# Kernel optimization log

Measured on AMD Instinct MI355X. Metric: run time of the kernel, lower is better.

The kernel has to match this reference:

```python
import jax, jax.numpy as jnp
import numpy as np

ROPE_BASE = 10000.0


def _rope_tables(T, d, dtype):
    # inv_freq over even indices, emb = concat(freqs, freqs) -> [T, d]
    inv_freq = 1.0 / (ROPE_BASE ** (jnp.arange(0, d, 2, dtype=jnp.float32) / d))
    t = jnp.arange(T, dtype=jnp.float32)
    freqs = jnp.einsum('i,j->ij', t, inv_freq)          # [T, d/2]
    emb = jnp.concatenate([freqs, freqs], axis=-1)      # [T, d]
    return jnp.cos(emb).astype(dtype), jnp.sin(emb).astype(dtype)


def _rotate_half(x):
    d = x.shape[-1] // 2
    return jnp.concatenate([-x[..., d:], x[..., :d]], axis=-1)


def _apply_rope(x, cos, sin):
    # x: [B, T, H, Dh]; cos/sin: [T, Dh] broadcast over batch and heads
    c = cos[None, :, None, :]
    s = sin[None, :, None, :]
    return x * c + _rotate_half(x) * s


def setup_inputs() -> dict:
    key = jax.random.key(0)
    k1, k2, k3 = jax.random.split(key, 3)
    B, T, C = 2, 2048, 1024
    x = jax.random.normal(k1, (B, T, C), dtype=jnp.float32)
    # weights stored as [in, out] (transposed nn.Linear), scaled like torch init
    W_qkv = jax.random.normal(k2, (C, 3 * C), dtype=jnp.float32) * (C ** -0.5)
    W_proj = jax.random.normal(k3, (C, C), dtype=jnp.float32) * (C ** -0.5)
    return {'x': x, 'W_qkv': W_qkv, 'W_proj': W_proj}


def reference(x, W_qkv, W_proj):
    B, T, C = x.shape
    H = 16
    Dh = C // H
    qkv = x @ W_qkv                                   # [B, T, 3C]
    q, k, v = jnp.split(qkv, 3, axis=-1)
    q = q.reshape(B, T, H, Dh)
    k = k.reshape(B, T, H, Dh)
    v = v.reshape(B, T, H, Dh)
    cos, sin = _rope_tables(T, Dh, x.dtype)
    q = _apply_rope(q, cos, sin)
    k = _apply_rope(k, cos, sin)
    scale = 1.0 / jnp.sqrt(jnp.asarray(Dh, dtype=x.dtype))
    # causal SDPA: scores [B, H, T, T]
    scores = jnp.einsum('bqhd,bkhd->bhqk', q, k) * scale
    causal = jnp.tril(jnp.ones((T, T), dtype=bool))
    scores = jnp.where(causal[None, None], scores, jnp.asarray(-jnp.inf, dtype=scores.dtype))
    attn = jax.nn.softmax(scores, axis=-1)
    y = jnp.einsum('bhqk,bkhd->bqhd', attn, v).reshape(B, T, C)
    return y @ W_proj
```

## Files before the change

### kernel.cpp

```cpp
#include <hip/hip_runtime.h>
#include <cstdint>
#include <cstddef>

typedef __bf16 bf16;
typedef __bf16 bf16x2 __attribute__((ext_vector_type(2)));
typedef __bf16 bf16x8 __attribute__((ext_vector_type(8)));
typedef float  f32x4  __attribute__((ext_vector_type(4)));

#define G2L(src, dst)                                                          \
  __builtin_amdgcn_global_load_lds(                                            \
      (const __attribute__((address_space(1))) unsigned int*)(src),            \
      (__attribute__((address_space(3))) unsigned int*)(dst), 16, 0, 0)

__global__ void k_f32_to_bf16(const float* __restrict__ in, bf16* __restrict__ out, int n) {
  int i = (blockIdx.x * blockDim.x + threadIdx.x) * 8;
  if (i >= n) return;
  float4 a = *(const float4*)(in + i);
  float4 b = *(const float4*)(in + i + 4);
  bf16x8 o;
  o[0] = (bf16)a.x; o[1] = (bf16)a.y; o[2] = (bf16)a.z; o[3] = (bf16)a.w;
  o[4] = (bf16)b.x; o[5] = (bf16)b.y; o[6] = (bf16)b.z; o[7] = (bf16)b.w;
  *(bf16x8*)(out + i) = o;
}

__global__ void k_transpose_f32_bf16(const float* __restrict__ in, bf16* __restrict__ out,
                                     int R, int C) {
  __shared__ float tile[32][33];
  int c0 = blockIdx.x * 32, r0 = blockIdx.y * 32;
  int tx = threadIdx.x & 31, ty = threadIdx.x >> 5;
#pragma unroll
  for (int i = 0; i < 32; i += 8)
    tile[ty + i][tx] = in[(size_t)(r0 + ty + i) * C + c0 + tx];
  __syncthreads();
#pragma unroll
  for (int i = 0; i < 32; i += 8)
    out[(size_t)(c0 + ty + i) * R + r0 + tx] = (bf16)tile[tx][ty + i];
}

__global__ void k_rope_tables(float* __restrict__ cosT, float* __restrict__ sinT, int total) {
  int i = blockIdx.x * blockDim.x + threadIdx.x;
  if (i >= total) return;
  int t = i >> 5, j = i & 31;
  float inv = powf(10000.0f, -(float)j * (1.0f / 32.0f));
  float f = (float)t * inv;
  cosT[i] = cosf(f);
  sinT[i] = sinf(f);
}

__global__ void k_rope_qk(const bf16* __restrict__ qkv, const float* __restrict__ cosT,
                          const float* __restrict__ sinT, bf16* __restrict__ qr,
                          bf16* __restrict__ kr) {
  int i = blockIdx.x * blockDim.x + threadIdx.x;
  int j = i & 31;
  int h = (i >> 5) & 15;
  int t = (i >> 9) & 2047;
  int b = i >> 20;
  size_t base = (size_t)(b * 2048 + t) * 3072;
  float c = cosT[t * 32 + j], s = sinT[t * 32 + j];
  float qlo = (float)qkv[base + h * 64 + j];
  float qhi = (float)qkv[base + h * 64 + j + 32];
  float klo = (float)qkv[base + 1024 + h * 64 + j];
  float khi = (float)qkv[base + 1024 + h * 64 + j + 32];
  size_t ob = ((size_t)(b * 16 + h) * 2048 + t) * 64;
  qr[ob + j]      = (bf16)((qlo * c - qhi * s) * 0.125f);
  qr[ob + j + 32] = (bf16)((qhi * c + qlo * s) * 0.125f);
  kr[ob + j]      = (bf16)(klo * c - khi * s);
  kr[ob + j + 32] = (bf16)(khi * c + klo * s);
}

__global__ void k_v_scatter(const bf16* __restrict__ qkv, bf16* __restrict__ vt) {
  __shared__ bf16 tile[64][66];
  int bh = blockIdx.y;
  int t0 = blockIdx.x * 64;
  int b = bh >> 4, h = bh & 15;
  int tt = threadIdx.x >> 2, c4 = (threadIdx.x & 3) * 16;
  const bf16* src = qkv + (size_t)(b * 2048 + t0 + tt) * 3072 + 2048 + h * 64 + c4;
  bf16x8 v0 = *(const bf16x8*)src;
  bf16x8 v1 = *(const bf16x8*)(src + 8);
#pragma unroll
  for (int j = 0; j < 8; j++) { tile[tt][c4 + j] = v0[j]; tile[tt][c4 + 8 + j] = v1[j]; }
  __syncthreads();
  int d = threadIdx.x >> 2, tc0 = (threadIdx.x & 3) * 16;
  bf16x8 o0, o1;
#pragma unroll
  for (int j = 0; j < 8; j++) { o0[j] = tile[tc0 + j][d]; o1[j] = tile[tc0 + 8 + j][d]; }
  bf16* dst = vt + ((size_t)bh * 64 + d) * 2048 + t0 + tc0;
  *(bf16x8*)dst = o0;
  *(bf16x8*)(dst + 8) = o1;
}

template <int OUTF32>
__global__ __launch_bounds__(256) void k_gemm_bt(const bf16* __restrict__ A,
                                                 const bf16* __restrict__ Bt,
                                                 float* __restrict__ Cf, bf16* __restrict__ Cb,
                                                 int M, int N, int K) {
  __shared__ __align__(16) bf16 sA[128 * 64];
  __shared__ __align__(16) bf16 sB[128 * 64];
  int m0 = blockIdx.y * 128, n0 = blockIdx.x * 128;
  int t = threadIdx.x, lane = t & 63, w = t >> 6;
  int wr = w >> 1, wc = w & 1;
  int lr = lane & 15, q2 = lane >> 4;
  int srow8 = lane >> 3, pc8 = lane & 7;
  f32x4 acc[4][4] = {};
  for (int k0 = 0; k0 < K; k0 += 64) {
#pragma unroll
    for (int is = 0; is < 4; is++) {
      int r = w * 32 + is * 8 + srow8;
      int lc = pc8 ^ (r & 7);
      G2L(A + (size_t)(m0 + r) * K + k0 + lc * 8, &sA[(w * 32 + is * 8) * 64]);
    }
#pragma unroll
    for (int is = 0; is < 4; is++) {
      int r = w * 32 + is * 8 + srow8;
      int lc = pc8 ^ (r & 7);
      G2L(Bt + (size_t)(n0 + r) * K + k0 + lc * 8, &sB[(w * 32 + is * 8) * 64]);
    }
    __syncthreads();
#pragma unroll
    for (int ch = 0; ch < 2; ch++) {
      bf16x8 af[4], bfr[4];
#pragma unroll
      for (int i = 0; i < 4; i++) {
        int r = wr * 64 + i * 16 + lr;
        af[i] = *(const bf16x8*)&sA[r * 64 + (((ch * 4 + q2) ^ (r & 7)) * 8)];
      }
#pragma unroll
      for (int i = 0; i < 4; i++) {
        int r = wc * 64 + i * 16 + lr;
        bfr[i] = *(const bf16x8*)&sB[r * 64 + (((ch * 4 + q2) ^ (r & 7)) * 8)];
      }
#pragma unroll
      for (int mi = 0; mi < 4; mi++)
#pragma unroll
        for (int ni = 0; ni < 4; ni++)
          acc[mi][ni] = __builtin_amdgcn_mfma_f32_16x16x32_bf16(af[mi], bfr[ni], acc[mi][ni], 0, 0, 0);
    }
    __syncthreads();
  }
  int row_base = m0 + wr * 64, col_base = n0 + wc * 64;
#pragma unroll
  for (int mi = 0; mi < 4; mi++)
#pragma unroll
    for (int ni = 0; ni < 4; ni++) {
      int col = col_base + ni * 16 + lr;
#pragma unroll
      for (int r = 0; r < 4; r++) {
        int row = row_base + mi * 16 + q2 * 4 + r;
        float v = acc[mi][ni][r];
        if (OUTF32) Cf[(size_t)row * N + col] = v;
        else        Cb[(size_t)row * N + col] = (bf16)v;
      }
    }
}

__global__ __launch_bounds__(256) void k_flash(const bf16* __restrict__ qr,
                                               const bf16* __restrict__ kr,
                                               const bf16* __restrict__ vt,
                                               bf16* __restrict__ out) {
  const int T = 2048;
  int pair = blockIdx.x;
  int bh = blockIdx.y;
  int b = bh >> 4, h = bh & 15;
  __shared__ __align__(16) bf16 sK[2][64 * 64];
  __shared__ __align__(16) bf16 sV[2][64 * 64];
  __shared__ __align__(16) bf16 sP[64][72];
  int t = threadIdx.x, lane = t & 63, w = t >> 6;
  int lr = lane & 15, q2 = lane >> 4;
  int srow8 = lane >> 3, pc8 = lane & 7;

  const bf16* Kbh = kr + (size_t)bh * T * 64;
  const bf16* Vbh = vt + (size_t)bh * 64 * T;

  for (int sel = 0; sel < 2; sel++) {
    int qt = sel ? 31 - pair : pair;
    int nk = qt + 1;
    const bf16* qrow = qr + ((size_t)bh * T + qt * 64 + w * 16 + lr) * 64;
    bf16x8 qf0 = *(const bf16x8*)(qrow + q2 * 8);
    bf16x8 qf1 = *(const bf16x8*)(qrow + 32 + q2 * 8);
    f32x4 o[4] = {};
    float m = -1e30f, l = 0.f;

    auto stage = [&](int buf, int kt) {
#pragma unroll
      for (int is = 0; is < 2; is++) {
        int r = w * 16 + is * 8 + srow8;
        int lc = pc8 ^ (r & 7);
        G2L(Kbh + (size_t)(kt * 64 + r) * 64 + lc * 8, &sK[buf][(w * 16 + is * 8) * 64]);
      }
#pragma unroll
      for (int is = 0; is < 2; is++) {
        int d = w * 16 + is * 8 + srow8;
        int lc = pc8 ^ (d & 7);
        G2L(Vbh + (size_t)d * T + kt * 64 + lc * 8, &sV[buf][(w * 16 + is * 8) * 64]);
      }
    };

    stage(0, 0);
    for (int kt = 0; kt < nk; kt++) {
      int buf = kt & 1;
      if (kt + 1 < nk) {
        stage(buf ^ 1, kt + 1);
        asm volatile("s_waitcnt vmcnt(4)" ::: "memory");
      } else {
        asm volatile("s_waitcnt vmcnt(0)" ::: "memory");
      }
      __builtin_amdgcn_s_barrier();
      asm volatile("" ::: "memory");
      __builtin_amdgcn_sched_barrier(0);
      const bf16* Kb = &sK[buf][0];
      const bf16* Vb = &sV[buf][0];
      f32x4 s[4];
#pragma unroll
      for (int kb = 0; kb < 4; kb++) {
        int rr = kb * 16 + lr;
        bf16x8 kf0 = *(const bf16x8*)&Kb[rr * 64 + ((q2 ^ (lr & 7)) * 8)];
        bf16x8 kf1 = *(const bf16x8*)&Kb[rr * 64 + (((4 + q2) ^ (lr & 7)) * 8)];
        f32x4 a = {};
        a = __builtin_amdgcn_mfma_f32_16x16x32_bf16(kf0, qf0, a, 0, 0, 0);
        a = __builtin_amdgcn_mfma_f32_16x16x32_bf16(kf1, qf1, a, 0, 0, 0);
        s[kb] = a;
      }
      if (kt == qt) {
#pragma unroll
        for (int kb = 0; kb < 4; kb++)
#pragma unroll
          for (int r = 0; r < 4; r++)
            if (kb * 16 + q2 * 4 + r > w * 16 + lr) s[kb][r] = -1e30f;
      }
      float px = -1e30f;
#pragma unroll
      for (int kb = 0; kb < 4; kb++)
#pragma unroll
        for (int r = 0; r < 4; r++) px = fmaxf(px, s[kb][r]);
      px = fmaxf(px, __shfl_xor(px, 16, 64));
      px = fmaxf(px, __shfl_xor(px, 32, 64));
      float mn = fmaxf(m, px);
      float alpha = __expf(m - mn);
      m = mn;
      float rs = 0.f;
#pragma unroll
      for (int kb = 0; kb < 4; kb++)
#pragma unroll
        for (int r = 0; r < 4; r++) {
          float p = __expf(s[kb][r] - m);
          s[kb][r] = p;
          rs += p;
        }
      rs += __shfl_xor(rs, 16, 64);
      rs += __shfl_xor(rs, 32, 64);
      l = l * alpha + rs;
#pragma unroll
      for (int kb = 0; kb < 4; kb++) {
        bf16x2 p01; p01[0] = (bf16)s[kb][0]; p01[1] = (bf16)s[kb][1];
        bf16x2 p23; p23[0] = (bf16)s[kb][2]; p23[1] = (bf16)s[kb][3];
        *(bf16x2*)&sP[w * 16 + lr][kb * 16 + q2 * 4]     = p01;
        *(bf16x2*)&sP[w * 16 + lr][kb * 16 + q2 * 4 + 2] = p23;
      }
      float ar[4];
#pragma unroll
      for (int r = 0; r < 4; r++) ar[r] = __shfl(alpha, q2 * 4 + r, 64);
#pragma unroll
      for (int db = 0; db < 4; db++)
#pragma unroll
        for (int r = 0; r < 4; r++) o[db][r] *= ar[r];
#pragma unroll
      for (int kh = 0; kh < 2; kh++) {
        bf16x8 pa = *(const bf16x8*)&sP[w * 16 + lr][kh * 32 + q2 * 8];
#pragma unroll
        for (int db = 0; db < 4; db++) {
          int dd = db * 16 + lr;
          bf16x8 vb = *(const bf16x8*)&Vb[dd * 64 + (((kh * 4 + q2) ^ (lr & 7)) * 8)];
          o[db] = __builtin_amdgcn_mfma_f32_16x16x32_bf16(pa, vb, o[db], 0, 0, 0);
        }
      }
      asm volatile("" ::: "memory");
      __builtin_amdgcn_s_barrier();
      asm volatile("" ::: "memory");
    }
    float linv[4];
#pragma unroll
    for (int r = 0; r < 4; r++) linv[r] = 1.0f / __shfl(l, q2 * 4 + r, 64);
#pragma unroll
    for (int db = 0; db < 4; db++)
#pragma unroll
      for (int r = 0; r < 4; r++) {
        int q = qt * 64 + w * 16 + q2 * 4 + r;
        out[((size_t)b * T + q) * 1024 + h * 64 + db * 16 + lr] = (bf16)(o[db][r] * linv[r]);
      }
  }
}

extern "C" void kernel_launch(void* const* d_in, const int* in_sizes, int n_in,
                              void* d_out, int out_size, void* d_ws, size_t ws_size,
                              hipStream_t stream) {
  const float* x     = (const float*)d_in[0];
  const float* Wqkv  = (const float*)d_in[1];
  const float* Wproj = (const float*)d_in[2];
  float* outp = (float*)d_out;
  const int B = 2, T = 2048, C = 1024;
  const int M = B * T;

  char* ws = (char*)d_ws;
  size_t off = 0;
  auto alloc = [&](size_t bytes) {
    void* p = ws + off;
    off += (bytes + 255) & ~(size_t)255;
    return p;
  };
  bf16* xb     = (bf16*)alloc((size_t)M * C * 2);
  bf16* wqkvt  = (bf16*)alloc((size_t)3 * C * C * 2);
  bf16* wprojt = (bf16*)alloc((size_t)C * C * 2);
  float* cosT  = (float*)alloc((size_t)T * 32 * 4);
  float* sinT  = (float*)alloc((size_t)T * 32 * 4);
  bf16* qkv    = (bf16*)alloc((size_t)M * 3 * C * 2);
  bf16* qr     = (bf16*)alloc((size_t)M * C * 2);
  bf16* kr     = (bf16*)alloc((size_t)M * C * 2);
  bf16* vt     = (bf16*)alloc((size_t)M * C * 2);
  bf16* attn   = qkv;

  k_f32_to_bf16<<<dim3(M * C / 8 / 256), dim3(256), 0, stream>>>(x, xb, M * C);
  k_transpose_f32_bf16<<<dim3(3 * C / 32, C / 32), dim3(256), 0, stream>>>(Wqkv, wqkvt, C, 3 * C);
  k_transpose_f32_bf16<<<dim3(C / 32, C / 32), dim3(256), 0, stream>>>(Wproj, wprojt, C, C);
  k_rope_tables<<<dim3(T * 32 / 256), dim3(256), 0, stream>>>(cosT, sinT, T * 32);
  k_gemm_bt<0><<<dim3(3 * C / 128, M / 128), dim3(256), 0, stream>>>(xb, wqkvt, (float*)nullptr, qkv, M, 3 * C, C);
  k_rope_qk<<<dim3((B * T * 16 * 32) / 256), dim3(256), 0, stream>>>(qkv, cosT, sinT, qr, kr);
  k_v_scatter<<<dim3(T / 64, 32), dim3(256), 0, stream>>>(qkv, vt);
  k_flash<<<dim3(16, 32), dim3(256), 0, stream>>>(qr, kr, vt, attn);
  k_gemm_bt<1><<<dim3(C / 128, M / 128), dim3(256), 0, stream>>>(attn, wprojt, outp, (bf16*)nullptr, M, C, C);
}
```

Measured before the change: 138.7 us.

## Enlarge flash-attention query tile to 128 using 32x32x16 MFMA per warp

Each flash block now handles a 128-row query tile, with each warp owning 32 query rows, instead of a 64-row tile with 16 rows per warp. Scores and PV use 32x32x16 bf16 MFMA with per-warp P buffers, and warps whose rows are fully masked skip the work for a key tile. The goal is to halve K/V staging per query row and raise MFMA efficiency. In exchange the grid shrinks to 256 blocks, which may underfill the GPU, and register pressure rises from the 32-wide accumulators.

```diff
diff --git a/kernel.cpp b/kernel.cpp
--- a/kernel.cpp
+++ b/kernel.cpp
@@ -4,8 +4,10 @@
 
 typedef __bf16 bf16;
 typedef __bf16 bf16x2 __attribute__((ext_vector_type(2)));
+typedef __bf16 bf16x4 __attribute__((ext_vector_type(4)));
 typedef __bf16 bf16x8 __attribute__((ext_vector_type(8)));
 typedef float  f32x4  __attribute__((ext_vector_type(4)));
+typedef float  f32x16 __attribute__((ext_vector_type(16)));
 
 #define G2L(src, dst)                                                          \
   __builtin_amdgcn_global_load_lds(                                            \
@@ -163,37 +165,41 @@
   int b = bh >> 4, h = bh & 15;
   __shared__ __align__(16) bf16 sK[2][64 * 64];
   __shared__ __align__(16) bf16 sV[2][64 * 64];
-  __shared__ __align__(16) bf16 sP[64][72];
+  __shared__ __align__(16) bf16 sP[4][32 * 68];
   int t = threadIdx.x, lane = t & 63, w = t >> 6;
-  int lr = lane & 15, q2 = lane >> 4;
+  int q31 = lane & 31, hi = lane >> 5;
   int srow8 = lane >> 3, pc8 = lane & 7;
+  bf16* Pw = &sP[w][0];
 
   const bf16* Kbh = kr + (size_t)bh * T * 64;
   const bf16* Vbh = vt + (size_t)bh * 64 * T;
 
+  auto stage = [&](int buf, int kt) {
+#pragma unroll
+    for (int is = 0; is < 2; is++) {
+      int r = w * 16 + is * 8 + srow8;
+      int lc = pc8 ^ (r & 7);
+      G2L(Kbh + (size_t)(kt * 64 + r) * 64 + lc * 8, &sK[buf][(w * 16 + is * 8) * 64]);
+    }
+#pragma unroll
+    for (int is = 0; is < 2; is++) {
+      int d = w * 16 + is * 8 + srow8;
+      int lc = pc8 ^ (d & 7);
+      G2L(Vbh + (size_t)d * T + kt * 64 + lc * 8, &sV[buf][(w * 16 + is * 8) * 64]);
+    }
+  };
+
   for (int sel = 0; sel < 2; sel++) {
-    int qt = sel ? 31 - pair : pair;
-    int nk = qt + 1;
-    const bf16* qrow = qr + ((size_t)bh * T + qt * 64 + w * 16 + lr) * 64;
-    bf16x8 qf0 = *(const bf16x8*)(qrow + q2 * 8);
-    bf16x8 qf1 = *(const bf16x8*)(qrow + 32 + q2 * 8);
-    f32x4 o[4] = {};
+    int qb = sel ? 15 - pair : pair;
+    int nk = 2 * qb + 2;
+    int qwb = qb * 128 + w * 32;
+    int qg = qwb + q31;
+    const bf16* qrow = qr + ((size_t)bh * T + qg) * 64 + hi * 8;
+    bf16x8 qf[4];
+#pragma unroll
+    for (int ks = 0; ks < 4; ks++) qf[ks] = *(const bf16x8*)(qrow + ks * 16);
+    f32x16 o0 = {}, o1 = {};
     float m = -1e30f, l = 0.f;
-
-    auto stage = [&](int buf, int kt) {
-#pragma unroll
-      for (int is = 0; is < 2; is++) {
-        int r = w * 16 + is * 8 + srow8;
-        int lc = pc8 ^ (r & 7);
-        G2L(Kbh + (size_t)(kt * 64 + r) * 64 + lc * 8, &sK[buf][(w * 16 + is * 8) * 64]);
-      }
-#pragma unroll
-      for (int is = 0; is < 2; is++) {
-        int d = w * 16 + is * 8 + srow8;
-        int lc = pc8 ^ (d & 7);
-        G2L(Vbh + (size_t)d * T + kt * 64 + lc * 8, &sV[buf][(w * 16 + is * 8) * 64]);
-      }
-    };
 
     stage(0, 0);
     for (int kt = 0; kt < nk; kt++) {
@@ -207,86 +213,100 @@
       __builtin_amdgcn_s_barrier();
       asm volatile("" ::: "memory");
       __builtin_amdgcn_sched_barrier(0);
-      const bf16* Kb = &sK[buf][0];
-      const bf16* Vb = &sV[buf][0];
-      f32x4 s[4];
-#pragma unroll
-      for (int kb = 0; kb < 4; kb++) {
-        int rr = kb * 16 + lr;
-        bf16x8 kf0 = *(const bf16x8*)&Kb[rr * 64 + ((q2 ^ (lr & 7)) * 8)];
-        bf16x8 kf1 = *(const bf16x8*)&Kb[rr * 64 + (((4 + q2) ^ (lr & 7)) * 8)];
-        f32x4 a = {};
-        a = __builtin_amdgcn_mfma_f32_16x16x32_bf16(kf0, qf0, a, 0, 0, 0);
-        a = __builtin_amdgcn_mfma_f32_16x16x32_bf16(kf1, qf1, a, 0, 0, 0);
-        s[kb] = a;
-      }
-      if (kt == qt) {
-#pragma unroll
-        for (int kb = 0; kb < 4; kb++)
-#pragma unroll
-          for (int r = 0; r < 4; r++)
-            if (kb * 16 + q2 * 4 + r > w * 16 + lr) s[kb][r] = -1e30f;
-      }
-      float px = -1e30f;
-#pragma unroll
-      for (int kb = 0; kb < 4; kb++)
-#pragma unroll
-        for (int r = 0; r < 4; r++) px = fmaxf(px, s[kb][r]);
-      px = fmaxf(px, __shfl_xor(px, 16, 64));
-      px = fmaxf(px, __shfl_xor(px, 32, 64));
-      float mn = fmaxf(m, px);
-      float alpha = __expf(m - mn);
-      m = mn;
-      float rs = 0.f;
-#pragma unroll
-      for (int kb = 0; kb < 4; kb++)
-#pragma unroll
-        for (int r = 0; r < 4; r++) {
-          float p = __expf(s[kb][r] - m);
-          s[kb][r] = p;
-          rs += p;
+      bool active = (kt * 64 <= qwb + 31);
+      if (active) {
+        const bf16* Kb = &sK[buf][0];
+        const bf16* Vb = &sV[buf][0];
+        f32x16 s[2];
+#pragma unroll
+        for (int kb = 0; kb < 2; kb++) {
+          f32x16 a = {};
+          int krow = kb * 32 + q31;
+#pragma unroll
+          for (int ks = 0; ks < 4; ks++) {
+            int ch = (ks * 2 + hi) ^ (krow & 7);
+            bf16x8 kf = *(const bf16x8*)&Kb[krow * 64 + ch * 8];
+            a = __builtin_amdgcn_mfma_f32_32x32x16_bf16(kf, qf[ks], a, 0, 0, 0);
+          }
+          s[kb] = a;
         }
-      rs += __shfl_xor(rs, 16, 64);
-      rs += __shfl_xor(rs, 32, 64);
-      l = l * alpha + rs;
-#pragma unroll
-      for (int kb = 0; kb < 4; kb++) {
-        bf16x2 p01; p01[0] = (bf16)s[kb][0]; p01[1] = (bf16)s[kb][1];
-        bf16x2 p23; p23[0] = (bf16)s[kb][2]; p23[1] = (bf16)s[kb][3];
-        *(bf16x2*)&sP[w * 16 + lr][kb * 16 + q2 * 4]     = p01;
-        *(bf16x2*)&sP[w * 16 + lr][kb * 16 + q2 * 4 + 2] = p23;
-      }
-      float ar[4];
-#pragma unroll
-      for (int r = 0; r < 4; r++) ar[r] = __shfl(alpha, q2 * 4 + r, 64);
-#pragma unroll
-      for (int db = 0; db < 4; db++)
-#pragma unroll
-        for (int r = 0; r < 4; r++) o[db][r] *= ar[r];
-#pragma unroll
-      for (int kh = 0; kh < 2; kh++) {
-        bf16x8 pa = *(const bf16x8*)&sP[w * 16 + lr][kh * 32 + q2 * 8];
-#pragma unroll
-        for (int db = 0; db < 4; db++) {
-          int dd = db * 16 + lr;
-          bf16x8 vb = *(const bf16x8*)&Vb[dd * 64 + (((kh * 4 + q2) ^ (lr & 7)) * 8)];
-          o[db] = __builtin_amdgcn_mfma_f32_16x16x32_bf16(pa, vb, o[db], 0, 0, 0);
+        if (kt * 64 + 63 > qwb) {
+          int thr = qg - kt * 64;
+#pragma unroll
+          for (int kb = 0; kb < 2; kb++)
+#pragma unroll
+            for (int r = 0; r < 16; r++) {
+              int koff = kb * 32 + (r & 3) + 8 * (r >> 2) + 4 * hi;
+              if (koff > thr) s[kb][r] = -1e30f;
+            }
+        }
+        float px = -1e30f;
+#pragma unroll
+        for (int kb = 0; kb < 2; kb++)
+#pragma unroll
+          for (int r = 0; r < 16; r++) px = fmaxf(px, s[kb][r]);
+        px = fmaxf(px, __shfl_xor(px, 32, 64));
+        float mn = fmaxf(m, px);
+        float alpha = __expf(m - mn);
+        m = mn;
+        float rs = 0.f;
+#pragma unroll
+        for (int kb = 0; kb < 2; kb++)
+#pragma unroll
+          for (int r = 0; r < 16; r++) {
+            float p = __expf(s[kb][r] - m);
+            s[kb][r] = p;
+            rs += p;
+          }
+        rs += __shfl_xor(rs, 32, 64);
+        l = l * alpha + rs;
+#pragma unroll
+        for (int kb = 0; kb < 2; kb++)
+#pragma unroll
+          for (int g = 0; g < 4; g++) {
+            bf16x4 pk;
+            pk[0] = (bf16)s[kb][4 * g + 0];
+            pk[1] = (bf16)s[kb][4 * g + 1];
+            pk[2] = (bf16)s[kb][4 * g + 2];
+            pk[3] = (bf16)s[kb][4 * g + 3];
+            *(bf16x4*)&Pw[q31 * 68 + kb * 32 + 8 * g + 4 * hi] = pk;
+          }
+#pragma unroll
+        for (int r = 0; r < 16; r++) { o0[r] *= alpha; o1[r] *= alpha; }
+#pragma unroll
+        for (int ks = 0; ks < 4; ks++) {
+          bf16x8 pb = *(const bf16x8*)&Pw[q31 * 68 + ks * 16 + hi * 8];
+          {
+            int drow = q31;
+            int ch = (ks * 2 + hi) ^ (drow & 7);
+            bf16x8 vf = *(const bf16x8*)&Vb[drow * 64 + ch * 8];
+            o0 = __builtin_amdgcn_mfma_f32_32x32x16_bf16(vf, pb, o0, 0, 0, 0);
+          }
+          {
+            int drow = 32 + q31;
+            int ch = (ks * 2 + hi) ^ (drow & 7);
+            bf16x8 vf = *(const bf16x8*)&Vb[drow * 64 + ch * 8];
+            o1 = __builtin_amdgcn_mfma_f32_32x32x16_bf16(vf, pb, o1, 0, 0, 0);
+          }
         }
       }
       asm volatile("" ::: "memory");
       __builtin_amdgcn_s_barrier();
       asm volatile("" ::: "memory");
     }
-    float linv[4];
-#pragma unroll
-    for (int r = 0; r < 4; r++) linv[r] = 1.0f / __shfl(l, q2 * 4 + r, 64);
-#pragma unroll
-    for (int db = 0; db < 4; db++)
-#pragma unroll
-      for (int r = 0; r < 4; r++) {
-        int q = qt * 64 + w * 16 + q2 * 4 + r;
-        out[((size_t)b * T + q) * 1024 + h * 64 + db * 16 + lr] = (bf16)(o[db][r] * linv[r]);
-      }
+    float linv = 1.0f / l;
+    bf16* orow = out + ((size_t)b * T + qg) * 1024 + h * 64;
+#pragma unroll
+    for (int g = 0; g < 4; g++) {
+      bf16x4 v0, v1;
+#pragma unroll
+      for (int j = 0; j < 4; j++) {
+        v0[j] = (bf16)(o0[4 * g + j] * linv);
+        v1[j] = (bf16)(o1[4 * g + j] * linv);
+      }
+      *(bf16x4*)&orow[8 * g + 4 * hi]      = v0;
+      *(bf16x4*)&orow[32 + 8 * g + 4 * hi] = v1;
+    }
   }
 }
 
@@ -325,6 +345,6 @@
   k_gemm_bt<0><<<dim3(3 * C / 128, M / 128), dim3(256), 0, stream>>>(xb, wqkvt, (float*)nullptr, qkv, M, 3 * C, C);
   k_rope_qk<<<dim3((B * T * 16 * 32) / 256), dim3(256), 0, stream>>>(qkv, cosT, sinT, qr, kr);
   k_v_scatter<<<dim3(T / 64, 32), dim3(256), 0, stream>>>(qkv, vt);
-  k_flash<<<dim3(16, 32), dim3(256), 0, stream>>>(qr, kr, vt, attn);
+  k_flash<<<dim3(8, 32), dim3(256), 0, stream>>>(qr, kr, vt, attn);
   k_gemm_bt<1><<<dim3(C / 128, M / 128), dim3(256), 0, stream>>>(attn, wprojt, outp, (bf16*)nullptr, M, C, C);
 }
```

New measurement: 153.0 us. +10.3%, slower.
